# Performance work log

Hardware: AMD Instinct MI355X
Metric: run time of the kernel (lower is better)

The kernel has to match this reference:

```python
import jax, jax.numpy as jnp
import numpy as np
import math

C = 1.0          # Poincare ball curvature
MIN_NORM = 1e-15
BALL_EPS = 1e-5  # clamp for artanh args


def _norm(x):
    return jnp.sqrt(jnp.maximum(jnp.sum(x * x, -1, keepdims=True), MIN_NORM))


def expmap0(u, c=C):
    sc = jnp.sqrt(c)
    n = _norm(u)
    return jnp.tanh(sc * n) * u / (sc * n)


def logmap0(x, c=C):
    sc = jnp.sqrt(c)
    n = _norm(x)
    return jnp.arctanh(jnp.minimum(sc * n, 1.0 - BALL_EPS)) * x / (sc * n)


def mobius_add(x, y, c=C):
    x2 = jnp.sum(x * x, -1, keepdims=True)
    y2 = jnp.sum(y * y, -1, keepdims=True)
    xy = jnp.sum(x * y, -1, keepdims=True)
    num = (1.0 + 2.0 * c * xy + c * y2) * x + (1.0 - c * x2) * y
    den = 1.0 + 2.0 * c * xy + c * c * x2 * y2
    return num / jnp.maximum(den, MIN_NORM)


def mobius_matvec(W, x, c=C):
    # W: (out, in), x: (..., in)
    sc = jnp.sqrt(c)
    xn = _norm(x)
    mx = x @ W.T
    mxn = _norm(mx)
    return jnp.tanh(mxn / xn * jnp.arctanh(jnp.minimum(sc * xn, 1.0 - BALL_EPS))) * mx / (mxn * sc)


def mobius_scalar_mul(r, x, c=C):
    sc = jnp.sqrt(c)
    n = _norm(x)
    return jnp.tanh(r * jnp.arctanh(jnp.minimum(sc * n, 1.0 - BALL_EPS))) * x / (n * sc)


def hyp_linear(x, W, b):
    return mobius_add(mobius_matvec(W, x), b)


def layer_norm(t, w, b, eps=1e-5):
    mu = jnp.mean(t, -1, keepdims=True)
    var = jnp.mean((t - mu) ** 2, -1, keepdims=True)
    return (t - mu) / jnp.sqrt(var + eps) * w + b


def hyp_layer_norm(x, w, b):
    return expmap0(layer_norm(logmap0(x), w, b))


def _hyperbolic_attention_scores(q, k, c=C, epsilon=1e-15, delta=1e-7):
    # q, k: (B, H, S, Dh)
    max_norm = (1.0 - 1e-5) / math.sqrt(c)
    q = jnp.minimum(q, max_norm)  # elementwise clamp_max, faithful to torch
    k = jnp.minimum(k, max_norm)
    q_norm_sq = c * jnp.sum(q * q, -1, keepdims=True)          # (B,H,Sq,1)
    k_norm_sq = c * jnp.sum(k * k, -1, keepdims=True)          # (B,H,Sk,1)
    # diff: (B,H,Sq,Sk,Dh) = mobius_add(-k, q) pairwise
    diff = mobius_add(-k[:, :, None, :, :], q[:, :, :, None, :], c)
    diff_norm_sq = c * jnp.sum(diff * diff, -1)                # (B,H,Sq,Sk)
    denom = (1.0 - q_norm_sq) * (1.0 - jnp.swapaxes(k_norm_sq, 2, 3)) + epsilon
    acosh_arg = 1.0 + 2.0 * diff_norm_sq / denom
    acosh_arg = jnp.maximum(acosh_arg, 1.0 + delta)
    dist = jnp.log(acosh_arg + jnp.sqrt(acosh_arg * acosh_arg - 1.0))
    return -dist


def setup_inputs() -> dict:
    key = jax.random.key(0)
    D, H, FF = 768, 12, 4 * 768
    B, S = 2, 196
    ks = jax.random.split(key, 8)

    def xavier(k, out_f, in_f):
        lim = math.sqrt(6.0 / (in_f + out_f))
        return jax.random.uniform(k, (out_f, in_f), jnp.float32, -lim, lim)

    x = jax.random.normal(ks[0], (B, S, D), jnp.float32) * 0.02  # inside unit ball
    return {
        "x": x,
        "wq": xavier(ks[1], D, D), "bq": jnp.zeros((D,), jnp.float32),
        "wk": xavier(ks[2], D, D), "bk": jnp.zeros((D,), jnp.float32),
        "wv": xavier(ks[3], D, D), "bv": jnp.zeros((D,), jnp.float32),
        "wo": xavier(ks[4], D, D), "bo": jnp.zeros((D,), jnp.float32),
        "head_scaling": jnp.ones((H, 1, 1), jnp.float32),
        "w1": xavier(ks[5], FF, D), "b1": jnp.zeros((FF,), jnp.float32),
        "w2": xavier(ks[6], D, FF), "b2": jnp.zeros((D,), jnp.float32),
        "beta": jnp.ones((1,), jnp.float32),
        "ln1_w": jnp.ones((D,), jnp.float32), "ln1_b": jnp.zeros((D,), jnp.float32),
        "ln2_w": jnp.ones((D,), jnp.float32), "ln2_b": jnp.zeros((D,), jnp.float32),
    }


def reference(x, wq, bq, wk, bk, wv, bv, wo, bo, head_scaling,
              w1, b1, w2, b2, beta, ln1_w, ln1_b, ln2_w, ln2_b):
    B, S, D = x.shape
    H = head_scaling.shape[0]
    Dh = D // H

    # --- hyperbolic multi-head attention ---
    q = hyp_linear(x, wq, bq)
    k = hyp_linear(x, wk, bk)
    v = hyp_linear(x, wv, bv)
    q = jnp.transpose(q.reshape(B, S, H, Dh), (0, 2, 1, 3))
    k = jnp.transpose(k.reshape(B, S, H, Dh), (0, 2, 1, 3))
    v = jnp.transpose(v.reshape(B, S, H, Dh), (0, 2, 1, 3))

    scores = _hyperbolic_attention_scores(q, k) / (head_scaling * math.sqrt(Dh))
    attn = jax.nn.softmax(scores, axis=-1)                       # (B,H,Sq,Sk)
    attn_out = expmap0(jnp.einsum('bhqk,bhkd->bhqd', attn, logmap0(v)))
    attn_out = jnp.transpose(attn_out, (0, 2, 1, 3)).reshape(B, S, D)
    attn_out = hyp_linear(attn_out, wo, bo)

    # --- residual 1 + hyperbolic layer norm ---
    h = mobius_add(x, mobius_scalar_mul(beta, attn_out))
    h = hyp_layer_norm(h, ln1_w, ln1_b)

    # --- mobius FFN ---
    f = hyp_linear(h, w1, b1)
    f = expmap0(jax.nn.relu(logmap0(f)))   # mobius_relu
    f = hyp_linear(f, w2, b2)

    # --- residual 2 + hyperbolic layer norm ---
    out = mobius_add(h, mobius_scalar_mul(beta, f))
    out = hyp_layer_norm(out, ln2_w, ln2_b)
    return out
```

## Files before the change

### kernel.cpp

```cpp
#include <hip/hip_runtime.h>
#include <hip/hip_bf16.h>
#include <math.h>

#define BATCH 2
#define SEQ 196
#define DMODEL 768
#define NHEAD 12
#define DHEAD 64
#define DFF 3072
#define NROWS (BATCH*SEQ)
#define NBH   (BATCH*NHEAD)
#define NHROWS (NBH*SEQ)

typedef __attribute__((ext_vector_type(8))) short short8;
typedef __attribute__((ext_vector_type(4))) float f32x4;

#define XB_OFF   0
#define XB_LEN   (NROWS*DMODEL)
#define WQ_OFF   (XB_OFF + XB_LEN)
#define WD_LEN   (DMODEL*DMODEL)
#define WK_OFF   (WQ_OFF + WD_LEN)
#define WV_OFF   (WK_OFF + WD_LEN)
#define WO_OFF   (WV_OFF + WD_LEN)
#define W1_OFF   (WO_OFF + WD_LEN)
#define WF_LEN   (DFF*DMODEL)
#define W2_OFF   (W1_OFF + WF_LEN)
#define BF_TOTAL (W2_OFF + WF_LEN)

__device__ __forceinline__ short f2bf(float f) {
  unsigned u = __builtin_bit_cast(unsigned, f);
  u += 0x7FFFu + ((u >> 16) & 1u);
  return (short)(u >> 16);
}
__device__ __forceinline__ float bf2f(short s) {
  unsigned u = ((unsigned)(unsigned short)s) << 16;
  return __builtin_bit_cast(float, u);
}
__device__ __forceinline__ float wave_sum64(float v) {
  #pragma unroll
  for (int off = 32; off; off >>= 1) v += __shfl_xor(v, off);
  return v;
}

__device__ __forceinline__ void block_reduce_sum4(float& a, float& b, float& c, float& d,
                                                  float* sbuf ) {
  #pragma unroll
  for (int off = 32; off; off >>= 1) {
    a += __shfl_xor(a, off);
    b += __shfl_xor(b, off);
    c += __shfl_xor(c, off);
    d += __shfl_xor(d, off);
  }
  int wid = threadIdx.x >> 6;
  if ((threadIdx.x & 63) == 0) {
    sbuf[wid*4+0] = a; sbuf[wid*4+1] = b; sbuf[wid*4+2] = c; sbuf[wid*4+3] = d;
  }
  __syncthreads();
  a = sbuf[0] + sbuf[4] + sbuf[8]  + sbuf[12];
  b = sbuf[1] + sbuf[5] + sbuf[9]  + sbuf[13];
  c = sbuf[2] + sbuf[6] + sbuf[10] + sbuf[14];
  d = sbuf[3] + sbuf[7] + sbuf[11] + sbuf[15];
  __syncthreads();
}

__global__ __launch_bounds__(256) void cvt_bf16(
    const float* __restrict__ x,  const float* __restrict__ wq,
    const float* __restrict__ wk, const float* __restrict__ wv,
    const float* __restrict__ wo, const float* __restrict__ w1,
    const float* __restrict__ w2, short* __restrict__ d) {
  const float* s; size_t n, o;
  switch (blockIdx.y) {
    case 0: s = x;  n = XB_LEN; o = XB_OFF; break;
    case 1: s = wq; n = WD_LEN; o = WQ_OFF; break;
    case 2: s = wk; n = WD_LEN; o = WK_OFF; break;
    case 3: s = wv; n = WD_LEN; o = WV_OFF; break;
    case 4: s = wo; n = WD_LEN; o = WO_OFF; break;
    case 5: s = w1; n = WF_LEN; o = W1_OFF; break;
    default: s = w2; n = WF_LEN; o = W2_OFF; break;
  }
  size_t units = n >> 3;
  for (size_t u = (size_t)blockIdx.x*256 + threadIdx.x; u < units; u += (size_t)gridDim.x*256) {
    const f32x4* sp = (const f32x4*)(s + u*8);
    f32x4 v0 = sp[0], v1 = sp[1];
    short8 r;
    #pragma unroll
    for (int j = 0; j < 4; ++j) { r[j] = f2bf(v0[j]); r[j+4] = f2bf(v1[j]); }
    *(short8*)(d + o + u*8) = r;
  }
}

#define PITCH 72
__global__ __launch_bounds__(256) void gemm_bf16(
    const short* __restrict__ X,
    const short* __restrict__ W1p, const short* __restrict__ W2p, const short* __restrict__ W3p,
    float* __restrict__ Y1, float* __restrict__ Y2, float* __restrict__ Y3,
    int n, int K, int m) {
  const short* W = W1p; float* Y = Y1;
  if (blockIdx.z == 1) { W = W2p; Y = Y2; }
  else if (blockIdx.z == 2) { W = W3p; Y = Y3; }

  __shared__ short As[64*PITCH];
  __shared__ short Bs[64*PITCH];
  const int tid  = threadIdx.x;
  const int lane = tid & 63;
  const int w    = tid >> 6, wr = w >> 1, wc = w & 1;
  const int brow = blockIdx.y * 64, bcol = blockIdx.x * 64;

  const int sr = tid >> 2, sc = (tid & 3) * 16;
  const bool rok = (brow + sr) < n;
  const short* xp = X + (size_t)(brow + sr) * K + sc;
  const short* wp = W + (size_t)(bcol + sr) * K + sc;

  f32x4 acc[2][2] = {};
  const int kgo = (lane >> 4) * 8;
  const short8 zero8 = {0,0,0,0,0,0,0,0};

  short8 xa0, xa1, wa0, wa1;
  if (rok) { xa0 = *(const short8*)(xp); xa1 = *(const short8*)(xp + 8); }
  else     { xa0 = zero8; xa1 = zero8; }
  wa0 = *(const short8*)(wp); wa1 = *(const short8*)(wp + 8);

  const int T = K / 64;
  for (int t = 0; t < T; ++t) {
    short8 xn0, xn1, wn0, wn1;
    const int kn = (t + 1 < T) ? (t + 1) * 64 : 0;
    if (rok) { xn0 = *(const short8*)(xp + kn); xn1 = *(const short8*)(xp + kn + 8); }
    else     { xn0 = zero8; xn1 = zero8; }
    wn0 = *(const short8*)(wp + kn); wn1 = *(const short8*)(wp + kn + 8);

    __syncthreads();
    *(short8*)&As[sr*PITCH + sc]     = xa0;
    *(short8*)&As[sr*PITCH + sc + 8] = xa1;
    *(short8*)&Bs[sr*PITCH + sc]     = wa0;
    *(short8*)&Bs[sr*PITCH + sc + 8] = wa1;
    __syncthreads();

    #pragma unroll
    for (int kk = 0; kk < 2; ++kk) {
      short8 a0 = *(const short8*)&As[(wr*32      + (lane & 15))*PITCH + kk*32 + kgo];
      short8 a1 = *(const short8*)&As[(wr*32 + 16 + (lane & 15))*PITCH + kk*32 + kgo];
      short8 b0 = *(const short8*)&Bs[(wc*32      + (lane & 15))*PITCH + kk*32 + kgo];
      short8 b1 = *(const short8*)&Bs[(wc*32 + 16 + (lane & 15))*PITCH + kk*32 + kgo];
      acc[0][0] = __builtin_amdgcn_mfma_f32_16x16x32_bf16(a0, b0, acc[0][0], 0, 0, 0);
      acc[0][1] = __builtin_amdgcn_mfma_f32_16x16x32_bf16(a0, b1, acc[0][1], 0, 0, 0);
      acc[1][0] = __builtin_amdgcn_mfma_f32_16x16x32_bf16(a1, b0, acc[1][0], 0, 0, 0);
      acc[1][1] = __builtin_amdgcn_mfma_f32_16x16x32_bf16(a1, b1, acc[1][1], 0, 0, 0);
    }
    xa0 = xn0; xa1 = xn1; wa0 = wn0; wa1 = wn1;
  }

  const int ccol = bcol + wc*32 + (lane & 15);
  #pragma unroll
  for (int mr = 0; mr < 2; ++mr) {
    #pragma unroll
    for (int j = 0; j < 4; ++j) {
      int grow = brow + wr*32 + mr*16 + (lane >> 4)*4 + j;
      if (grow < n) {
        float* yr = Y + (size_t)grow * m + ccol;
        yr[0]  = acc[mr][0][j];
        yr[16] = acc[mr][1][j];
      }
    }
  }
}

#define P_P 256
__global__ __launch_bounds__(256) void qkv_post(const float* __restrict__ X,
                                                const float* __restrict__ MQ,
                                                const float* __restrict__ MK,
                                                const float* __restrict__ MV,
                                                const float* __restrict__ bq,
                                                const float* __restrict__ bk,
                                                const float* __restrict__ bv,
                                                short* __restrict__ qhb,
                                                short* __restrict__ khb,
                                                float* __restrict__ q2s,
                                                float* __restrict__ k2s,
                                                short* __restrict__ lvT) {
  __shared__ float sbuf[16];
  const int r = blockIdx.x;
  const int b = r / SEQ, s = r % SEQ;
  const int y = blockIdx.y;
  const float* MX   = (y == 0) ? MQ : (y == 1) ? MK : MV;
  const float* bias = (y == 0) ? bq : (y == 1) ? bk : bv;
  const float* xr = X + (size_t)r*DMODEL;
  const float* mr = MX + (size_t)r*DMODEL;
  const int tid = threadIdx.x, wid = tid >> 6, lane = tid & 63;
  const float maxn = 1.0f - 1e-5f;

  float xs = 0.f, ms = 0.f, mb = 0.f, bb = 0.f;
  float mv[3], bvv[3];
  #pragma unroll
  for (int l = 0; l < 3; ++l) {
    int i = tid + l*256;
    float xv = xr[i];
    mv[l] = mr[i]; bvv[l] = bias[i];
    xs += xv*xv; ms += mv[l]*mv[l]; mb += mv[l]*bvv[l]; bb += bvv[l]*bvv[l];
  }
  block_reduce_sum4(xs, ms, mb, bb, sbuf);
  float xn  = sqrtf(fmaxf(xs, 1e-15f));
  float mxn = sqrtf(fmaxf(ms, 1e-15f));
  float art = atanhf(fminf(xn, maxn));
  float scm = tanhf(mxn/xn*art)/mxn;
  float x2 = scm*scm*ms;
  float y2 = bb;
  float xy = scm*mb;
  float den = fmaxf(1.f + 2.f*xy + x2*y2, 1e-15f);
  float ca = (1.f + 2.f*xy + y2) * scm / den;
  float cb = (1.f - x2) / den;

  #pragma unroll
  for (int l = 0; l < 3; ++l) {
    float o = ca*mv[l] + cb*bvv[l];
    int h = l*4 + wid;
    size_t hr = (size_t)(b*NHEAD + h)*SEQ + s;
    if (y < 2) {
      short c16 = f2bf(fminf(o, maxn));
      float cf = bf2f(c16);
      float nn = wave_sum64(cf*cf);
      if (y == 0) {
        qhb[hr*64 + lane] = c16;
        if (lane == 0) q2s[hr] = nn;
      } else {
        khb[hr*64 + lane] = c16;
        if (lane == 0) k2s[hr] = nn;
      }
    } else {
      float nn = wave_sum64(o*o);
      float n = sqrtf(fmaxf(nn, 1e-15f));
      float scl = atanhf(fminf(n, maxn))/n;
      lvT[((size_t)(b*NHEAD + h)*DHEAD + lane)*P_P + s] = f2bf(scl*o);
    }
  }
}

#define SP 72
#define PP 264
__global__ __launch_bounds__(256) void attn_mfma(
    const short* __restrict__ qhb, const short* __restrict__ khb,
    const float* __restrict__ q2s, const float* __restrict__ k2s,
    const short* __restrict__ lvT, const float* __restrict__ hs,
    float* __restrict__ ao, short* __restrict__ aob) {
  __shared__ __align__(16) char smem[9216 + 224*SP*2];
  __shared__ float q2l[64];
  __shared__ float k2l[224];
  __shared__ float redA[64][2];
  __shared__ float redB[64][2];

  const int tile = blockIdx.x, bh = blockIdx.z;
  const int h = bh % NHEAD, b = bh / NHEAD;
  const int i0 = tile*64;
  const int tid = threadIdx.x, lane = tid & 63, w = tid >> 6, wr = w >> 1, wc = w & 1;
  short* Qs = (short*)smem;
  short* Ks = (short*)(smem + 9216);
  short* Pl = (short*)smem;
  const short8 z8 = {0,0,0,0,0,0,0,0};
  const int kgo = (lane >> 4)*8;

  {
    int row = tid >> 2, seg = (tid & 3)*16;
    int gr = i0 + row;
    short8 v0 = z8, v1 = z8;
    if (gr < SEQ) {
      const short* p = qhb + ((size_t)bh*SEQ + gr)*64 + seg;
      v0 = *(const short8*)p; v1 = *(const short8*)(p + 8);
    }
    *(short8*)&Qs[row*SP + seg]     = v0;
    *(short8*)&Qs[row*SP + seg + 8] = v1;
  }
  for (int u = tid; u < 224*4; u += 256) {
    int row = u >> 2, seg = (u & 3)*16;
    short8 v0 = z8, v1 = z8;
    if (row < SEQ) {
      const short* p = khb + ((size_t)bh*SEQ + row)*64 + seg;
      v0 = *(const short8*)p; v1 = *(const short8*)(p + 8);
    }
    *(short8*)&Ks[row*SP + seg]     = v0;
    *(short8*)&Ks[row*SP + seg + 8] = v1;
  }
  if (tid < 64)  q2l[tid] = (i0 + tid < SEQ) ? q2s[(size_t)bh*SEQ + i0 + tid] : 0.f;
  if (tid < 224) k2l[tid] = (tid < SEQ) ? k2s[(size_t)bh*SEQ + tid] : 0.f;
  __syncthreads();

  f32x4 acc[2][7] = {};
  #pragma unroll
  for (int kk = 0; kk < 2; ++kk) {
    short8 a0 = *(const short8*)&Qs[(wr*32      + (lane & 15))*SP + kk*32 + kgo];
    short8 a1 = *(const short8*)&Qs[(wr*32 + 16 + (lane & 15))*SP + kk*32 + kgo];
    #pragma unroll
    for (int cf = 0; cf < 7; ++cf) {
      short8 bf = *(const short8*)&Ks[(wc*112 + cf*16 + (lane & 15))*SP + kk*32 + kgo];
      acc[0][cf] = __builtin_amdgcn_mfma_f32_16x16x32_bf16(a0, bf, acc[0][cf], 0, 0, 0);
      acc[1][cf] = __builtin_amdgcn_mfma_f32_16x16x32_bf16(a1, bf, acc[1][cf], 0, 0, 0);
    }
  }

  const float inv_hsv = 1.f/(hs[h]*8.0f);
  #pragma unroll
  for (int rf = 0; rf < 2; ++rf) {
    #pragma unroll
    for (int j = 0; j < 4; ++j) {
      int rl = wr*32 + rf*16 + (lane >> 4)*4 + j;
      float q2 = q2l[rl];
      #pragma unroll
      for (int cf = 0; cf < 7; ++cf) {
        int col = wc*112 + cf*16 + (lane & 15);
        float kq = acc[rf][cf][j];
        float k2 = k2l[col];
        float xy = -kq;
        float al = 1.f + 2.f*xy + q2;
        float be = 1.f - k2;
        float num2 = al*al*k2 + 2.f*al*be*xy + be*be*q2;
        float den  = fmaxf(1.f + 2.f*xy + k2*q2, 1e-15f);
        float dns  = num2/(den*den);
        float denom = (1.f - q2)*(1.f - k2) + 1e-15f;
        float arg = fmaxf(1.f + 2.f*dns/denom, 1.f + 1e-7f);
        float dist = logf(arg + sqrtf(arg*arg - 1.f));
        acc[rf][cf][j] = (col < SEQ) ? -dist*inv_hsv : -1e30f;
      }
      float m = acc[rf][0][j];
      #pragma unroll
      for (int cf = 1; cf < 7; ++cf) m = fmaxf(m, acc[rf][cf][j]);
      m = fmaxf(m, __shfl_xor(m, 1));
      m = fmaxf(m, __shfl_xor(m, 2));
      m = fmaxf(m, __shfl_xor(m, 4));
      m = fmaxf(m, __shfl_xor(m, 8));
      if ((lane & 15) == 0) redA[rl][wc] = m;
    }
  }
  __syncthreads();

  #pragma unroll
  for (int rf = 0; rf < 2; ++rf) {
    #pragma unroll
    for (int j = 0; j < 4; ++j) {
      int rl = wr*32 + rf*16 + (lane >> 4)*4 + j;
      float m = fmaxf(redA[rl][0], redA[rl][1]);
      float s = 0.f;
      #pragma unroll
      for (int cf = 0; cf < 7; ++cf) {
        float e = expf(acc[rf][cf][j] - m);
        acc[rf][cf][j] = e;
        s += e;
      }
      s += __shfl_xor(s, 1); s += __shfl_xor(s, 2);
      s += __shfl_xor(s, 4); s += __shfl_xor(s, 8);
      if ((lane & 15) == 0) redB[rl][wc] = s;
    }
  }
  __syncthreads();

  #pragma unroll
  for (int rf = 0; rf < 2; ++rf) {
    #pragma unroll
    for (int j = 0; j < 4; ++j) {
      int rl = wr*32 + rf*16 + (lane >> 4)*4 + j;
      float inv = 1.f/(redB[rl][0] + redB[rl][1]);
      #pragma unroll
      for (int cf = 0; cf < 7; ++cf) {
        int col = wc*112 + cf*16 + (lane & 15);
        Pl[rl*PP + col] = f2bf(acc[rf][cf][j]*inv);
      }
    }
  }
  __syncthreads();

  f32x4 acc2[2][2] = {};
  const short* lvb = lvT + (size_t)bh*DHEAD*P_P;
  #pragma unroll
  for (int ks = 0; ks < 7; ++ks) {
    short8 a0 = *(const short8*)&Pl[(wr*32      + (lane & 15))*PP + ks*32 + kgo];
    short8 a1 = *(const short8*)&Pl[(wr*32 + 16 + (lane & 15))*PP + ks*32 + kgo];
    short8 b0 = *(const short8*)(lvb + (size_t)(wc*32      + (lane & 15))*P_P + ks*32 + kgo);
    short8 b1 = *(const short8*)(lvb + (size_t)(wc*32 + 16 + (lane & 15))*P_P + ks*32 + kgo);
    acc2[0][0] = __builtin_amdgcn_mfma_f32_16x16x32_bf16(a0, b0, acc2[0][0], 0, 0, 0);
    acc2[0][1] = __builtin_amdgcn_mfma_f32_16x16x32_bf16(a0, b1, acc2[0][1], 0, 0, 0);
    acc2[1][0] = __builtin_amdgcn_mfma_f32_16x16x32_bf16(a1, b0, acc2[1][0], 0, 0, 0);
    acc2[1][1] = __builtin_amdgcn_mfma_f32_16x16x32_bf16(a1, b1, acc2[1][1], 0, 0, 0);
  }

  #pragma unroll
  for (int rf = 0; rf < 2; ++rf) {
    #pragma unroll
    for (int j = 0; j < 4; ++j) {
      int rl = wr*32 + rf*16 + (lane >> 4)*4 + j;
      float s = acc2[rf][0][j]*acc2[rf][0][j] + acc2[rf][1][j]*acc2[rf][1][j];
      s += __shfl_xor(s, 1); s += __shfl_xor(s, 2);
      s += __shfl_xor(s, 4); s += __shfl_xor(s, 8);
      if ((lane & 15) == 0) redA[rl][wc] = s;
    }
  }
  __syncthreads();

  #pragma unroll
  for (int rf = 0; rf < 2; ++rf) {
    #pragma unroll
    for (int j = 0; j < 4; ++j) {
      int rl = wr*32 + rf*16 + (lane >> 4)*4 + j;
      int grow = i0 + rl;
      if (grow < SEQ) {
        float n2 = redA[rl][0] + redA[rl][1];
        float n = sqrtf(fmaxf(n2, 1e-15f));
        float scl = tanhf(n)/n;
        #pragma unroll
        for (int cf2 = 0; cf2 < 2; ++cf2) {
          int col = h*64 + wc*32 + cf2*16 + (lane & 15);
          float o = scl*acc2[rf][cf2][j];
          size_t idx = (size_t)(b*SEQ + grow)*DMODEL + col;
          ao[idx] = o;
          aob[idx] = f2bf(o);
        }
      }
    }
  }
}

__global__ __launch_bounds__(256) void post_resid_ln(
    const float* __restrict__ Xfull, const float* __restrict__ xsArr, int din,
    const float* __restrict__ MX, const float* __restrict__ bias,
    const float* __restrict__ RX,
    const float* __restrict__ betap, const float* __restrict__ lnw,
    const float* __restrict__ lnb,
    float* __restrict__ out, short* __restrict__ outb) {
  __shared__ float sbuf[16];
  const int r = blockIdx.x;
  const int tid = threadIdx.x;
  const float* mr = MX + (size_t)r*DMODEL;

  float xs = 0.f, ms = 0.f, mb = 0.f, bb = 0.f;
  float mv[3], bvv[3];
  #pragma unroll
  for (int l = 0; l < 3; ++l) {
    int i = tid + l*256;
    mv[l] = mr[i]; bvv[l] = bias[i];
    ms += mv[l]*mv[l]; mb += mv[l]*bvv[l]; bb += bvv[l]*bvv[l];
  }
  if (Xfull) {
    const float* xr = Xfull + (size_t)r*din;
    for (int i = tid; i < din; i += 256) { float v = xr[i]; xs += v*v; }
  }
  block_reduce_sum4(xs, ms, mb, bb, sbuf);
  if (!Xfull) xs = xsArr[r];

  float xn  = sqrtf(fmaxf(xs, 1e-15f));
  float mxn = sqrtf(fmaxf(ms, 1e-15f));
  float art = atanhf(fminf(xn, 1.f - 1e-5f));
  float scm = tanhf(mxn/xn*art)/mxn;
  float px2 = scm*scm*ms;
  float py2 = bb;
  float pxy = scm*mb;
  float pden = fmaxf(1.f + 2.f*pxy + px2*py2, 1e-15f);
  float pca = (1.f + 2.f*pxy + py2) * scm / pden;
  float pcb = (1.f - px2) / pden;

  const float* xr2 = RX + (size_t)r*DMODEL;
  float xv[3], yv[3];
  float x2 = 0.f, xy = 0.f, d1 = 0.f, d2 = 0.f;
  #pragma unroll
  for (int l = 0; l < 3; ++l) {
    int i = tid + l*256;
    xv[l] = xr2[i];
    yv[l] = pca*mv[l] + pcb*bvv[l];
    x2 += xv[l]*xv[l]; xy += xv[l]*yv[l];
  }
  block_reduce_sum4(x2, xy, d1, d2, sbuf);
  float yy = pca*pca*ms + 2.f*pca*pcb*mb + pcb*pcb*bb;

  float beta = betap[0];
  float ny = sqrtf(fmaxf(yy, 1e-15f));
  float scs = tanhf(beta * atanhf(fminf(ny, 1.f - 1e-5f))) / ny;
  float y2  = scs*scs*yy;
  float xys = scs*xy;
  float den = fmaxf(1.f + 2.f*xys + x2*y2, 1e-15f);
  float ca = (1.f + 2.f*xys + y2)/den;
  float cb = (1.f - x2)*scs/den;
  float hv[3]; float h2 = 0.f;
  #pragma unroll
  for (int l = 0; l < 3; ++l) { hv[l] = ca*xv[l] + cb*yv[l]; h2 += hv[l]*hv[l]; }
  float z1 = 0.f, z2 = 0.f, z3 = 0.f;
  block_reduce_sum4(h2, z1, z2, z3, sbuf);

  float nh = sqrtf(fmaxf(h2, 1e-15f));
  float scl = atanhf(fminf(nh, 1.f - 1e-5f))/nh;
  float tv[3]; float tsum = 0.f, tsq = 0.f;
  #pragma unroll
  for (int l = 0; l < 3; ++l) { tv[l] = scl*hv[l]; tsum += tv[l]; tsq += tv[l]*tv[l]; }
  float zz = 0.f, zw = 0.f;
  block_reduce_sum4(tsum, tsq, zz, zw, sbuf);
  float mu  = tsum * (1.f/768.f);
  float var = tsq * (1.f/768.f) - mu*mu;
  float rstd = rsqrtf(var + 1e-5f);
  float lnv[3]; float l2 = 0.f;
  #pragma unroll
  for (int l = 0; l < 3; ++l) {
    int i = tid + l*256;
    lnv[l] = (tv[l] - mu)*rstd*lnw[i] + lnb[i];
    l2 += lnv[l]*lnv[l];
  }
  float w1 = 0.f, w2 = 0.f, w3 = 0.f;
  block_reduce_sum4(l2, w1, w2, w3, sbuf);
  float nl = sqrtf(fmaxf(l2, 1e-15f));
  float sce = tanhf(nl)/nl;
  #pragma unroll
  for (int l = 0; l < 3; ++l) {
    int i = tid + l*256;
    float o = sce*lnv[l];
    out[(size_t)r*DMODEL + i] = o;
    if (outb) outb[(size_t)r*DMODEL + i] = f2bf(o);
  }
}

__global__ __launch_bounds__(256) void ffn1_post(const float* __restrict__ hb,
                                                 const float* __restrict__ MX,
                                                 const float* __restrict__ bias,
                                                 short* __restrict__ fbb,
                                                 float* __restrict__ fnorm) {
  __shared__ float sbuf[16];
  const int r = blockIdx.x;
  const int tid = threadIdx.x;
  const float* xr = hb + (size_t)r*DMODEL;
  const float* mr = MX + (size_t)r*DFF;

  float xs = 0.f, ms = 0.f, mb = 0.f, bb = 0.f;
  float mv[12], bvv[12];
  for (int i = tid; i < DMODEL; i += 256) { float v = xr[i]; xs += v*v; }
  #pragma unroll
  for (int l = 0; l < 12; ++l) {
    int i = tid + l*256;
    mv[l] = mr[i]; bvv[l] = bias[i];
    ms += mv[l]*mv[l]; mb += mv[l]*bvv[l]; bb += bvv[l]*bvv[l];
  }
  block_reduce_sum4(xs, ms, mb, bb, sbuf);
  float xn  = sqrtf(fmaxf(xs, 1e-15f));
  float mxn = sqrtf(fmaxf(ms, 1e-15f));
  float art = atanhf(fminf(xn, 1.f - 1e-5f));
  float scm = tanhf(mxn/xn*art)/mxn;
  float px2 = scm*scm*ms;
  float py2 = bb;
  float pxy = scm*mb;
  float pden = fmaxf(1.f + 2.f*pxy + px2*py2, 1e-15f);
  float pca = (1.f + 2.f*pxy + py2) * scm / pden;
  float pcb = (1.f - px2) / pden;

  float s2 = pca*pca*ms + 2.f*pca*pcb*mb + pcb*pcb*bb;
  float n = sqrtf(fmaxf(s2, 1e-15f));
  float scl = atanhf(fminf(n, 1.f - 1e-5f))/n;
  float rv[12]; float r2 = 0.f;
  #pragma unroll
  for (int l = 0; l < 12; ++l) {
    float f = pca*mv[l] + pcb*bvv[l];
    rv[l] = fmaxf(scl*f, 0.f);
    r2 += rv[l]*rv[l];
  }
  float w1 = 0.f, w2 = 0.f, w3 = 0.f;
  block_reduce_sum4(r2, w1, w2, w3, sbuf);
  float nr = sqrtf(fmaxf(r2, 1e-15f));
  float sce = tanhf(nr)/nr;
  #pragma unroll
  for (int l = 0; l < 12; ++l)
    fbb[(size_t)r*DFF + tid + l*256] = f2bf(sce*rv[l]);
  if (tid == 0) fnorm[r] = sce*sce*r2;
}

extern "C" void kernel_launch(void* const* d_in, const int* in_sizes, int n_in,
                              void* d_out, int out_size, void* d_ws, size_t ws_size,
                              hipStream_t stream) {
  const float* x    = (const float*)d_in[0];
  const float* wq   = (const float*)d_in[1];
  const float* bq   = (const float*)d_in[2];
  const float* wk   = (const float*)d_in[3];
  const float* bk   = (const float*)d_in[4];
  const float* wv   = (const float*)d_in[5];
  const float* bv   = (const float*)d_in[6];
  const float* wo   = (const float*)d_in[7];
  const float* bo   = (const float*)d_in[8];
  const float* hs   = (const float*)d_in[9];
  const float* w1   = (const float*)d_in[10];
  const float* b1   = (const float*)d_in[11];
  const float* w2   = (const float*)d_in[12];
  const float* b2   = (const float*)d_in[13];
  const float* beta = (const float*)d_in[14];
  const float* ln1w = (const float*)d_in[15];
  const float* ln1b = (const float*)d_in[16];
  const float* ln2w = (const float*)d_in[17];
  const float* ln2b = (const float*)d_in[18];
  float* out = (float*)d_out;

  char* base = (char*)d_ws;
  size_t off = 0;
  auto allocB = [&](size_t bytes) {
    off = (off + 63) & ~(size_t)63;
    void* p = base + off; off += bytes; return p;
  };
  short* bfp  = (short*)allocB((size_t)BF_TOTAL * 2);
  short* aob  = (short*)allocB((size_t)NROWS*DMODEL * 2);
  short* hbb  = (short*)allocB((size_t)NROWS*DMODEL * 2);
  short* fbb  = (short*)allocB((size_t)NROWS*DFF * 2);
  float* tq   = (float*)allocB((size_t)NROWS*DMODEL * 4);
  float* tk   = (float*)allocB((size_t)NROWS*DMODEL * 4);
  float* tv   = (float*)allocB((size_t)NROWS*DMODEL * 4);
  short* qhb  = (short*)allocB((size_t)NHROWS*DHEAD * 2);
  short* khb  = (short*)allocB((size_t)NHROWS*DHEAD * 2);
  float* q2s  = (float*)allocB((size_t)NHROWS * 4);
  float* k2s  = (float*)allocB((size_t)NHROWS * 4);
  short* lvT  = (short*)allocB((size_t)NBH*DHEAD*P_P * 2);
  float* ao   = (float*)allocB((size_t)NROWS*DMODEL * 4);
  float* hb   = (float*)allocB((size_t)NROWS*DMODEL * 4);
  float* tmpF = (float*)allocB((size_t)NROWS*DFF * 4);
  float* fnorm= (float*)allocB((size_t)NROWS * 4);

  const short* xb  = bfp + XB_OFF;
  const short* wqb = bfp + WQ_OFF;
  const short* wkb = bfp + WK_OFF;
  const short* wvb = bfp + WV_OFF;
  const short* wob = bfp + WO_OFF;
  const short* w1b = bfp + W1_OFF;
  const short* w2b = bfp + W2_OFF;

  dim3 blk(256);
  dim3 gCVT(1152, 7);
  dim3 gQKV(DMODEL/64, (NROWS+63)/64, 3);
  dim3 gD(DMODEL/64,  (NROWS+63)/64, 1);
  dim3 gF(DFF/64,     (NROWS+63)/64, 1);
  dim3 gATT(4, 1, NBH);

  cvt_bf16<<<gCVT, blk, 0, stream>>>(x, wq, wk, wv, wo, w1, w2, bfp);

  gemm_bf16<<<gQKV, blk, 0, stream>>>(xb, wqb, wkb, wvb, tq, tk, tv, NROWS, DMODEL, DMODEL);
  qkv_post<<<dim3(NROWS, 3), blk, 0, stream>>>(x, tq, tk, tv, bq, bk, bv,
                                               qhb, khb, q2s, k2s, lvT);

  attn_mfma<<<gATT, blk, 0, stream>>>(qhb, khb, q2s, k2s, lvT, hs, ao, aob);

  gemm_bf16<<<gD, blk, 0, stream>>>(aob, wob, wob, wob, tq, tq, tq, NROWS, DMODEL, DMODEL);
  post_resid_ln<<<NROWS, blk, 0, stream>>>(ao, nullptr, DMODEL, tq, bo, x,
                                           beta, ln1w, ln1b, hb, hbb);

  gemm_bf16<<<gF, blk, 0, stream>>>(hbb, w1b, w1b, w1b, tmpF, tmpF, tmpF, NROWS, DMODEL, DFF);
  ffn1_post<<<NROWS, blk, 0, stream>>>(hb, tmpF, b1, fbb, fnorm);
  gemm_bf16<<<gD, blk, 0, stream>>>(fbb, w2b, w2b, w2b, tq, tq, tq, NROWS, DFF, DMODEL);
  post_resid_ln<<<NROWS, blk, 0, stream>>>(nullptr, fnorm, DFF, tq, b2, hb,
                                           beta, ln2w, ln2b, out, nullptr);
}
```

Before: 129.3 us.

## Fuse fp32-to-bf16 weight conversion into GEMM loads and split-K small GEMMs

Drops the separate conversion pass that wrote bf16 copies of x and all weights. The GEMMs now load fp32 operands and round them to bf16 in registers before staging to LDS, which removes one full read-write pass over the weights but doubles the bytes each GEMM reads. The out-projection and FFN2 GEMMs are split along K into 2 and 4 partial outputs that post_resid_ln sums, giving more blocks on the GPU. The fp32 attention output buffer is removed, so the norm is taken from the bf16 copy, which slightly changes precision.

```diff
diff --git a/kernel.cpp b/kernel.cpp
--- a/kernel.cpp
+++ b/kernel.cpp
@@ -15,18 +15,6 @@
 typedef __attribute__((ext_vector_type(8))) short short8;
 typedef __attribute__((ext_vector_type(4))) float f32x4;
 
-#define XB_OFF   0
-#define XB_LEN   (NROWS*DMODEL)
-#define WQ_OFF   (XB_OFF + XB_LEN)
-#define WD_LEN   (DMODEL*DMODEL)
-#define WK_OFF   (WQ_OFF + WD_LEN)
-#define WV_OFF   (WK_OFF + WD_LEN)
-#define WO_OFF   (WV_OFF + WD_LEN)
-#define W1_OFF   (WO_OFF + WD_LEN)
-#define WF_LEN   (DFF*DMODEL)
-#define W2_OFF   (W1_OFF + WF_LEN)
-#define BF_TOTAL (W2_OFF + WF_LEN)
-
 __device__ __forceinline__ short f2bf(float f) {
   unsigned u = __builtin_bit_cast(unsigned, f);
   u += 0x7FFFu + ((u >> 16) & 1u);
@@ -63,41 +51,16 @@
   __syncthreads();
 }
 
-__global__ __launch_bounds__(256) void cvt_bf16(
-    const float* __restrict__ x,  const float* __restrict__ wq,
-    const float* __restrict__ wk, const float* __restrict__ wv,
-    const float* __restrict__ wo, const float* __restrict__ w1,
-    const float* __restrict__ w2, short* __restrict__ d) {
-  const float* s; size_t n, o;
-  switch (blockIdx.y) {
-    case 0: s = x;  n = XB_LEN; o = XB_OFF; break;
-    case 1: s = wq; n = WD_LEN; o = WQ_OFF; break;
-    case 2: s = wk; n = WD_LEN; o = WK_OFF; break;
-    case 3: s = wv; n = WD_LEN; o = WV_OFF; break;
-    case 4: s = wo; n = WD_LEN; o = WO_OFF; break;
-    case 5: s = w1; n = WF_LEN; o = W1_OFF; break;
-    default: s = w2; n = WF_LEN; o = W2_OFF; break;
-  }
-  size_t units = n >> 3;
-  for (size_t u = (size_t)blockIdx.x*256 + threadIdx.x; u < units; u += (size_t)gridDim.x*256) {
-    const f32x4* sp = (const f32x4*)(s + u*8);
-    f32x4 v0 = sp[0], v1 = sp[1];
-    short8 r;
-    #pragma unroll
-    for (int j = 0; j < 4; ++j) { r[j] = f2bf(v0[j]); r[j+4] = f2bf(v1[j]); }
-    *(short8*)(d + o + u*8) = r;
-  }
-}
-
 #define PITCH 72
-__global__ __launch_bounds__(256) void gemm_bf16(
-    const short* __restrict__ X,
-    const short* __restrict__ W1p, const short* __restrict__ W2p, const short* __restrict__ W3p,
-    float* __restrict__ Y1, float* __restrict__ Y2, float* __restrict__ Y3,
-    int n, int K, int m) {
-  const short* W = W1p; float* Y = Y1;
-  if (blockIdx.z == 1) { W = W2p; Y = Y2; }
-  else if (blockIdx.z == 2) { W = W3p; Y = Y3; }
+
+__global__ __launch_bounds__(256) void gemm_qkv_f32(
+    const float* __restrict__ X,
+    const float* __restrict__ Wq, const float* __restrict__ Wk, const float* __restrict__ Wv,
+    float* __restrict__ Yq, float* __restrict__ Yk, float* __restrict__ Yv) {
+  const float* W = Wq; float* Y = Yq;
+  if (blockIdx.z == 1) { W = Wk; Y = Yk; }
+  else if (blockIdx.z == 2) { W = Wv; Y = Yv; }
+  const int K = DMODEL, m = DMODEL, n = NROWS;
 
   __shared__ short As[64*PITCH];
   __shared__ short Bs[64*PITCH];
@@ -108,31 +71,43 @@
 
   const int sr = tid >> 2, sc = (tid & 3) * 16;
   const bool rok = (brow + sr) < n;
-  const short* xp = X + (size_t)(brow + sr) * K + sc;
-  const short* wp = W + (size_t)(bcol + sr) * K + sc;
+  const float* xp = X + (size_t)(brow + sr) * K + sc;
+  const float* wp = W + (size_t)(bcol + sr) * K + sc;
 
   f32x4 acc[2][2] = {};
   const int kgo = (lane >> 4) * 8;
-  const short8 zero8 = {0,0,0,0,0,0,0,0};
-
-  short8 xa0, xa1, wa0, wa1;
-  if (rok) { xa0 = *(const short8*)(xp); xa1 = *(const short8*)(xp + 8); }
-  else     { xa0 = zero8; xa1 = zero8; }
-  wa0 = *(const short8*)(wp); wa1 = *(const short8*)(wp + 8);
+  const f32x4 zf = {0.f,0.f,0.f,0.f};
+
+  f32x4 xa[4], wa[4];
+  #pragma unroll
+  for (int q = 0; q < 4; ++q) {
+    xa[q] = rok ? *(const f32x4*)(xp + q*4) : zf;
+    wa[q] = *(const f32x4*)(wp + q*4);
+  }
 
   const int T = K / 64;
   for (int t = 0; t < T; ++t) {
-    short8 xn0, xn1, wn0, wn1;
+    f32x4 xn[4], wn[4];
     const int kn = (t + 1 < T) ? (t + 1) * 64 : 0;
-    if (rok) { xn0 = *(const short8*)(xp + kn); xn1 = *(const short8*)(xp + kn + 8); }
-    else     { xn0 = zero8; xn1 = zero8; }
-    wn0 = *(const short8*)(wp + kn); wn1 = *(const short8*)(wp + kn + 8);
-
+    #pragma unroll
+    for (int q = 0; q < 4; ++q) {
+      xn[q] = rok ? *(const f32x4*)(xp + kn + q*4) : zf;
+      wn[q] = *(const f32x4*)(wp + kn + q*4);
+    }
+
+    short8 xs0, xs1, ws0, ws1;
+    #pragma unroll
+    for (int j = 0; j < 4; ++j) {
+      xs0[j] = f2bf(xa[0][j]); xs0[j+4] = f2bf(xa[1][j]);
+      xs1[j] = f2bf(xa[2][j]); xs1[j+4] = f2bf(xa[3][j]);
+      ws0[j] = f2bf(wa[0][j]); ws0[j+4] = f2bf(wa[1][j]);
+      ws1[j] = f2bf(wa[2][j]); ws1[j+4] = f2bf(wa[3][j]);
+    }
     __syncthreads();
-    *(short8*)&As[sr*PITCH + sc]     = xa0;
-    *(short8*)&As[sr*PITCH + sc + 8] = xa1;
-    *(short8*)&Bs[sr*PITCH + sc]     = wa0;
-    *(short8*)&Bs[sr*PITCH + sc + 8] = wa1;
+    *(short8*)&As[sr*PITCH + sc]     = xs0;
+    *(short8*)&As[sr*PITCH + sc + 8] = xs1;
+    *(short8*)&Bs[sr*PITCH + sc]     = ws0;
+    *(short8*)&Bs[sr*PITCH + sc + 8] = ws1;
     __syncthreads();
 
     #pragma unroll
@@ -146,7 +121,93 @@
       acc[1][0] = __builtin_amdgcn_mfma_f32_16x16x32_bf16(a1, b0, acc[1][0], 0, 0, 0);
       acc[1][1] = __builtin_amdgcn_mfma_f32_16x16x32_bf16(a1, b1, acc[1][1], 0, 0, 0);
     }
-    xa0 = xn0; xa1 = xn1; wa0 = wn0; wa1 = wn1;
+    #pragma unroll
+    for (int q = 0; q < 4; ++q) { xa[q] = xn[q]; wa[q] = wn[q]; }
+  }
+
+  const int ccol = bcol + wc*32 + (lane & 15);
+  #pragma unroll
+  for (int mr = 0; mr < 2; ++mr) {
+    #pragma unroll
+    for (int j = 0; j < 4; ++j) {
+      int grow = brow + wr*32 + mr*16 + (lane >> 4)*4 + j;
+      if (grow < n) {
+        float* yr = Y + (size_t)grow * m + ccol;
+        yr[0]  = acc[mr][0][j];
+        yr[16] = acc[mr][1][j];
+      }
+    }
+  }
+}
+
+__global__ __launch_bounds__(256) void gemm_awf32(
+    const short* __restrict__ A, const float* __restrict__ W,
+    float* __restrict__ Yparts, int n, int Ktot, int m, int KK) {
+  const int z = blockIdx.z;
+  const int kbase = z * KK;
+  float* Y = Yparts + (size_t)z * n * m;
+
+  __shared__ short As[64*PITCH];
+  __shared__ short Bs[64*PITCH];
+  const int tid  = threadIdx.x;
+  const int lane = tid & 63;
+  const int w    = tid >> 6, wr = w >> 1, wc = w & 1;
+  const int brow = blockIdx.y * 64, bcol = blockIdx.x * 64;
+
+  const int sr = tid >> 2, sc = (tid & 3) * 16;
+  const bool rok = (brow + sr) < n;
+  const short* ap = A + (size_t)(brow + sr) * Ktot + kbase + sc;
+  const float* wp = W + (size_t)(bcol + sr) * Ktot + kbase + sc;
+
+  f32x4 acc[2][2] = {};
+  const int kgo = (lane >> 4) * 8;
+  const short8 z8 = {0,0,0,0,0,0,0,0};
+  const f32x4 zf = {0.f,0.f,0.f,0.f};
+
+  short8 aa0, aa1;
+  f32x4 wa[4];
+  if (rok) { aa0 = *(const short8*)(ap); aa1 = *(const short8*)(ap + 8); }
+  else     { aa0 = z8; aa1 = z8; }
+  #pragma unroll
+  for (int q = 0; q < 4; ++q) wa[q] = *(const f32x4*)(wp + q*4);
+
+  const int T = KK / 64;
+  for (int t = 0; t < T; ++t) {
+    short8 an0, an1;
+    f32x4 wn[4];
+    const int kn = (t + 1 < T) ? (t + 1) * 64 : 0;
+    if (rok) { an0 = *(const short8*)(ap + kn); an1 = *(const short8*)(ap + kn + 8); }
+    else     { an0 = z8; an1 = z8; }
+    #pragma unroll
+    for (int q = 0; q < 4; ++q) wn[q] = *(const f32x4*)(wp + kn + q*4);
+
+    short8 ws0, ws1;
+    #pragma unroll
+    for (int j = 0; j < 4; ++j) {
+      ws0[j] = f2bf(wa[0][j]); ws0[j+4] = f2bf(wa[1][j]);
+      ws1[j] = f2bf(wa[2][j]); ws1[j+4] = f2bf(wa[3][j]);
+    }
+    __syncthreads();
+    *(short8*)&As[sr*PITCH + sc]     = aa0;
+    *(short8*)&As[sr*PITCH + sc + 8] = aa1;
+    *(short8*)&Bs[sr*PITCH + sc]     = ws0;
+    *(short8*)&Bs[sr*PITCH + sc + 8] = ws1;
+    __syncthreads();
+
+    #pragma unroll
+    for (int kk = 0; kk < 2; ++kk) {
+      short8 a0 = *(const short8*)&As[(wr*32      + (lane & 15))*PITCH + kk*32 + kgo];
+      short8 a1 = *(const short8*)&As[(wr*32 + 16 + (lane & 15))*PITCH + kk*32 + kgo];
+      short8 b0 = *(const short8*)&Bs[(wc*32      + (lane & 15))*PITCH + kk*32 + kgo];
+      short8 b1 = *(const short8*)&Bs[(wc*32 + 16 + (lane & 15))*PITCH + kk*32 + kgo];
+      acc[0][0] = __builtin_amdgcn_mfma_f32_16x16x32_bf16(a0, b0, acc[0][0], 0, 0, 0);
+      acc[0][1] = __builtin_amdgcn_mfma_f32_16x16x32_bf16(a0, b1, acc[0][1], 0, 0, 0);
+      acc[1][0] = __builtin_amdgcn_mfma_f32_16x16x32_bf16(a1, b0, acc[1][0], 0, 0, 0);
+      acc[1][1] = __builtin_amdgcn_mfma_f32_16x16x32_bf16(a1, b1, acc[1][1], 0, 0, 0);
+    }
+    aa0 = an0; aa1 = an1;
+    #pragma unroll
+    for (int q = 0; q < 4; ++q) wa[q] = wn[q];
   }
 
   const int ccol = bcol + wc*32 + (lane & 15);
@@ -240,7 +301,7 @@
     const short* __restrict__ qhb, const short* __restrict__ khb,
     const float* __restrict__ q2s, const float* __restrict__ k2s,
     const short* __restrict__ lvT, const float* __restrict__ hs,
-    float* __restrict__ ao, short* __restrict__ aob) {
+    short* __restrict__ aob) {
   __shared__ __align__(16) char smem[9216 + 224*SP*2];
   __shared__ float q2l[64];
   __shared__ float k2l[224];
@@ -406,9 +467,7 @@
         for (int cf2 = 0; cf2 < 2; ++cf2) {
           int col = h*64 + wc*32 + cf2*16 + (lane & 15);
           float o = scl*acc2[rf][cf2][j];
-          size_t idx = (size_t)(b*SEQ + grow)*DMODEL + col;
-          ao[idx] = o;
-          aob[idx] = f2bf(o);
+          aob[(size_t)(b*SEQ + grow)*DMODEL + col] = f2bf(o);
         }
       }
     }
@@ -416,31 +475,33 @@
 }
 
 __global__ __launch_bounds__(256) void post_resid_ln(
-    const float* __restrict__ Xfull, const float* __restrict__ xsArr, int din,
-    const float* __restrict__ MX, const float* __restrict__ bias,
-    const float* __restrict__ RX,
+    const short* __restrict__ Xbf, const float* __restrict__ xsArr, int din,
+    const float* __restrict__ MXp, int nparts,
+    const float* __restrict__ bias, const float* __restrict__ RX,
     const float* __restrict__ betap, const float* __restrict__ lnw,
     const float* __restrict__ lnb,
     float* __restrict__ out, short* __restrict__ outb) {
   __shared__ float sbuf[16];
   const int r = blockIdx.x;
   const int tid = threadIdx.x;
-  const float* mr = MX + (size_t)r*DMODEL;
 
   float xs = 0.f, ms = 0.f, mb = 0.f, bb = 0.f;
   float mv[3], bvv[3];
   #pragma unroll
   for (int l = 0; l < 3; ++l) {
     int i = tid + l*256;
-    mv[l] = mr[i]; bvv[l] = bias[i];
+    float acc = 0.f;
+    for (int p = 0; p < nparts; ++p)
+      acc += MXp[(size_t)p*NROWS*DMODEL + (size_t)r*DMODEL + i];
+    mv[l] = acc; bvv[l] = bias[i];
     ms += mv[l]*mv[l]; mb += mv[l]*bvv[l]; bb += bvv[l]*bvv[l];
   }
-  if (Xfull) {
-    const float* xr = Xfull + (size_t)r*din;
-    for (int i = tid; i < din; i += 256) { float v = xr[i]; xs += v*v; }
+  if (Xbf) {
+    const short* xr = Xbf + (size_t)r*din;
+    for (int i = tid; i < din; i += 256) { float v = bf2f(xr[i]); xs += v*v; }
   }
   block_reduce_sum4(xs, ms, mb, bb, sbuf);
-  if (!Xfull) xs = xsArr[r];
+  if (!Xbf) xs = xsArr[r];
 
   float xn  = sqrtf(fmaxf(xs, 1e-15f));
   float mxn = sqrtf(fmaxf(ms, 1e-15f));
@@ -592,53 +653,42 @@
     off = (off + 63) & ~(size_t)63;
     void* p = base + off; off += bytes; return p;
   };
-  short* bfp  = (short*)allocB((size_t)BF_TOTAL * 2);
   short* aob  = (short*)allocB((size_t)NROWS*DMODEL * 2);
   short* hbb  = (short*)allocB((size_t)NROWS*DMODEL * 2);
   short* fbb  = (short*)allocB((size_t)NROWS*DFF * 2);
   float* tq   = (float*)allocB((size_t)NROWS*DMODEL * 4);
   float* tk   = (float*)allocB((size_t)NROWS*DMODEL * 4);
   float* tv   = (float*)allocB((size_t)NROWS*DMODEL * 4);
+  float* gparts = (float*)allocB((size_t)4*NROWS*DMODEL * 4);
   short* qhb  = (short*)allocB((size_t)NHROWS*DHEAD * 2);
   short* khb  = (short*)allocB((size_t)NHROWS*DHEAD * 2);
   float* q2s  = (float*)allocB((size_t)NHROWS * 4);
   float* k2s  = (float*)allocB((size_t)NHROWS * 4);
   short* lvT  = (short*)allocB((size_t)NBH*DHEAD*P_P * 2);
-  float* ao   = (float*)allocB((size_t)NROWS*DMODEL * 4);
   float* hb   = (float*)allocB((size_t)NROWS*DMODEL * 4);
   float* tmpF = (float*)allocB((size_t)NROWS*DFF * 4);
   float* fnorm= (float*)allocB((size_t)NROWS * 4);
 
-  const short* xb  = bfp + XB_OFF;
-  const short* wqb = bfp + WQ_OFF;
-  const short* wkb = bfp + WK_OFF;
-  const short* wvb = bfp + WV_OFF;
-  const short* wob = bfp + WO_OFF;
-  const short* w1b = bfp + W1_OFF;
-  const short* w2b = bfp + W2_OFF;
-
   dim3 blk(256);
-  dim3 gCVT(1152, 7);
   dim3 gQKV(DMODEL/64, (NROWS+63)/64, 3);
-  dim3 gD(DMODEL/64,  (NROWS+63)/64, 1);
-  dim3 gF(DFF/64,     (NROWS+63)/64, 1);
+  dim3 gO(DMODEL/64,   (NROWS+63)/64, 2);
+  dim3 gF1(DFF/64,     (NROWS+63)/64, 1);
+  dim3 gF2(DMODEL/64,  (NROWS+63)/64, 4);
   dim3 gATT(4, 1, NBH);
 
-  cvt_bf16<<<gCVT, blk, 0, stream>>>(x, wq, wk, wv, wo, w1, w2, bfp);
-
-  gemm_bf16<<<gQKV, blk, 0, stream>>>(xb, wqb, wkb, wvb, tq, tk, tv, NROWS, DMODEL, DMODEL);
+  gemm_qkv_f32<<<gQKV, blk, 0, stream>>>(x, wq, wk, wv, tq, tk, tv);
   qkv_post<<<dim3(NROWS, 3), blk, 0, stream>>>(x, tq, tk, tv, bq, bk, bv,
                                                qhb, khb, q2s, k2s, lvT);
 
-  attn_mfma<<<gATT, blk, 0, stream>>>(qhb, khb, q2s, k2s, lvT, hs, ao, aob);
-
-  gemm_bf16<<<gD, blk, 0, stream>>>(aob, wob, wob, wob, tq, tq, tq, NROWS, DMODEL, DMODEL);
-  post_resid_ln<<<NROWS, blk, 0, stream>>>(ao, nullptr, DMODEL, tq, bo, x,
+  attn_mfma<<<gATT, blk, 0, stream>>>(qhb, khb, q2s, k2s, lvT, hs, aob);
+
+  gemm_awf32<<<gO, blk, 0, stream>>>(aob, wo, gparts, NROWS, DMODEL, DMODEL, DMODEL/2);
+  post_resid_ln<<<NROWS, blk, 0, stream>>>(aob, nullptr, DMODEL, gparts, 2, bo, x,
                                            beta, ln1w, ln1b, hb, hbb);
 
-  gemm_bf16<<<gF, blk, 0, stream>>>(hbb, w1b, w1b, w1b, tmpF, tmpF, tmpF, NROWS, DMODEL, DFF);
+  gemm_awf32<<<gF1, blk, 0, stream>>>(hbb, w1, tmpF, NROWS, DMODEL, DFF, DMODEL);
   ffn1_post<<<NROWS, blk, 0, stream>>>(hb, tmpF, b1, fbb, fnorm);
-  gemm_bf16<<<gD, blk, 0, stream>>>(fbb, w2b, w2b, w2b, tq, tq, tq, NROWS, DFF, DMODEL);
-  post_resid_ln<<<NROWS, blk, 0, stream>>>(nullptr, fnorm, DFF, tq, b2, hb,
+  gemm_awf32<<<gF2, blk, 0, stream>>>(fbb, w2, gparts, NROWS, DFF, DMODEL, DFF/4);
+  post_resid_ln<<<NROWS, blk, 0, stream>>>(nullptr, fnorm, DFF, gparts, 4, b2, hb,
                                            beta, ln2w, ln2b, out, nullptr);
 }
```

Result: faster. 111.6 us (-13.7%).
